# Performance work log

Hardware: AMD Instinct MI355X
Metric: run time of the kernel (lower is better)

The kernel has to match this reference:

```python
import jax, jax.numpy as jnp
import numpy as np

B, C, T, K = 16, 512, 2048, 64

def setup_inputs() -> dict:
    key = jax.random.key(0)
    k1, k2, k3 = jax.random.split(key, 3)
    v = jax.random.normal(k1, (B, C, T), dtype=jnp.float32)
    # 1x1 Conv1d weights == linear maps over channel dim
    Wk = jax.random.normal(k2, (K, C), dtype=jnp.float32) * 0.02
    bk = jnp.zeros((K,), dtype=jnp.float32)
    Wq = jax.random.normal(k3, (K, C), dtype=jnp.float32) * 0.02
    bq = jnp.zeros((K,), dtype=jnp.float32)
    gamma = jnp.ones((), dtype=jnp.float32)
    return {"v": v, "Wk": Wk, "bk": bk, "Wq": Wq, "bq": bq, "gamma": gamma}

def reference(v, Wk, bk, Wq, bq, gamma):
    # k, q: (B, K, T) via 1x1 conv = channel-wise linear
    k = jnp.einsum('kc,bct->bkt', Wk, v) + bk[None, :, None]
    q = jnp.einsum('kc,bct->bkt', Wq, v) + bq[None, :, None]
    # original: e1[b,d,i,j]=q[b,d,j], e2[b,d,i,j]=k[b,d,i]; sum over d
    # -> s[b,i,j] = sum_d k[b,d,i] * q[b,d,j]  (avoid materializing B,K,T,T)
    s = jnp.einsum('bdi,bdj->bij', k, q)  # (B, T, T)
    a = jax.nn.softmax(s, axis=1)          # softmax over dim=1 (the i axis)
    att = jnp.einsum('bct,btj->bcj', v, a)  # bmm(v, a)
    return v + gamma * att
```

## Files before the change

### kernel.cpp

```cpp
#include <hip/hip_runtime.h>

#define Bc 16
#define Cc 512
#define Tc 2048
#define QT 128
#define KT 64
#define PST 72
#define LTS 66

typedef __attribute__((ext_vector_type(8))) short short8;
typedef __attribute__((ext_vector_type(4))) float f32x4;
typedef unsigned short u16;

static __device__ __forceinline__ u16 f2bf(float x) {
  unsigned u = __float_as_uint(x);
  u += 0x7FFF + ((u >> 16) & 1);
  return (u16)(u >> 16);
}

static __device__ __forceinline__ void block_sync_lds() {
  __builtin_amdgcn_sched_barrier(0);
  asm volatile("s_waitcnt lgkmcnt(0)" ::: "memory");
  __builtin_amdgcn_s_barrier();
  __builtin_amdgcn_sched_barrier(0);
}

__global__ __launch_bounds__(256) void prep_kernel(
    const float* __restrict__ Wk, const float* __restrict__ Wq,
    const float* __restrict__ bk, const float* __restrict__ bq,
    u16* __restrict__ Wbf, float* __restrict__ bkq)
{
  int idx  = blockIdx.x * 256 + threadIdx.x;
  int base = idx * 4;
  if (base < 128 * Cc) {
    int ch = base >> 9;
    int c  = base & (Cc - 1);
    const float* src = (ch < 64) ? (Wk + (size_t)ch * Cc + c)
                                 : (Wq + (size_t)(ch - 64) * Cc + c);
    f32x4 w = *reinterpret_cast<const f32x4*>(src);
    uint2 o;
    o.x = (unsigned)f2bf(w[0]) | ((unsigned)f2bf(w[1]) << 16);
    o.y = (unsigned)f2bf(w[2]) | ((unsigned)f2bf(w[3]) << 16);
    *reinterpret_cast<uint2*>(Wbf + base) = o;
  }
  if (idx < 128) bkq[idx] = (idx < 64) ? bk[idx] : bq[idx - 64];
}

__global__ __launch_bounds__(256) void kqv_kernel(
    const float* __restrict__ v, const u16* __restrict__ Wbf,
    const float* __restrict__ bkq, u16* __restrict__ kq, u16* __restrict__ vbf)
{
  __shared__ u16 LDSt[2][64][LTS];
  const int b   = blockIdx.y;
  const int t0  = blockIdx.x * 64;
  const int tid = threadIdx.x;
  const int lane = tid & 63;
  const int w    = tid >> 6;
  const int l15  = lane & 15;
  const int lg   = lane >> 4;

  f32x4 acc[8];
  #pragma unroll
  for (int mt = 0; mt < 8; ++mt) acc[mt] = f32x4{0.f, 0.f, 0.f, 0.f};

  const float* vb = v + (size_t)b * Cc * Tc + t0;
  float x[16];
  #pragma unroll
  for (int r = 0; r < 16; ++r) x[r] = vb[(size_t)(w * 16 + r) * Tc + lane];

  int buf = 0;
  for (int c0 = 0; c0 < Cc; c0 += 64, buf ^= 1) {
    #pragma unroll
    for (int r = 0; r < 16; ++r) {
      u16 hb = f2bf(x[r]);
      LDSt[buf][lane][w * 16 + r] = hb;
      vbf[((size_t)b * Cc + c0 + w * 16 + r) * Tc + t0 + lane] = hb;
    }
    block_sync_lds();
    if (c0 + 64 < Cc) {
      #pragma unroll
      for (int r = 0; r < 16; ++r)
        x[r] = vb[(size_t)(c0 + 64 + w * 16 + r) * Tc + lane];
    }
    #pragma unroll
    for (int ks = 0; ks < 2; ++ks) {
      short8 bfrag = *reinterpret_cast<const short8*>(&LDSt[buf][w * 16 + l15][ks * 32 + lg * 8]);
      #pragma unroll
      for (int mt = 0; mt < 8; ++mt) {
        short8 afrag = *reinterpret_cast<const short8*>(
            Wbf + (size_t)(mt * 16 + l15) * Cc + c0 + ks * 32 + lg * 8);
        acc[mt] = __builtin_amdgcn_mfma_f32_16x16x32_bf16(afrag, bfrag, acc[mt], 0, 0, 0);
      }
    }
  }
  const int t = t0 + w * 16 + l15;
  u16* op = kq + ((size_t)b * Tc + t) * 128;
  #pragma unroll
  for (int mt = 0; mt < 8; ++mt) {
    int chb = mt * 16 + lg * 4;
    float a0 = acc[mt][0] + bkq[chb + 0];
    float a1 = acc[mt][1] + bkq[chb + 1];
    float a2 = acc[mt][2] + bkq[chb + 2];
    float a3 = acc[mt][3] + bkq[chb + 3];
    uint2 o;
    o.x = (unsigned)f2bf(a0) | ((unsigned)f2bf(a1) << 16);
    o.y = (unsigned)f2bf(a2) | ((unsigned)f2bf(a3) << 16);
    *reinterpret_cast<uint2*>(op + chb) = o;
  }
}

__global__ __launch_bounds__(512, 2) void attn_kernel(
    const float* __restrict__ v, const u16* __restrict__ vbf,
    const u16* __restrict__ kq, const float* __restrict__ gamma_p,
    float* __restrict__ out)
{
  __shared__ u16 P[2][QT * PST];
  __shared__ float scl_lds[2][QT];
  __shared__ float lsum_lds[QT];

  const int L   = blockIdx.x;
  const int lin = (L & 7) * 32 + (L >> 3);
  const int b   = lin >> 4;
  const int j0  = (lin & 15) * QT;
  const int tid = threadIdx.x;
  const int lane = tid & 63;
  const int wid  = tid >> 6;
  const int l15  = lane & 15;
  const int lg   = lane >> 4;
  const int c0   = wid * 64;

  short8 qf0, qf1;
  {
    const u16* qp = kq + (size_t)(b * Tc + j0 + wid * 16 + l15) * 128 + 64 + lg * 8;
    qf0 = *reinterpret_cast<const short8*>(qp);
    qf1 = *reinterpret_cast<const short8*>(qp + 32);
  }

  f32x4 O[4][8];
  #pragma unroll
  for (int a = 0; a < 4; ++a)
    #pragma unroll
    for (int bb = 0; bb < 8; ++bb) O[a][bb] = f32x4{0.f, 0.f, 0.f, 0.f};

  float m = -1e30f, lsum = 0.f;

  const u16* kbase = kq + (size_t)b * Tc * 128 + lg * 8;
  const u16* vbase = vbf + ((size_t)b * Cc + c0) * Tc;

  short8 kf[4][2];
  short8 vf[2][4];
  #pragma unroll
  for (int it = 0; it < 4; ++it) {
    const u16* kp = kbase + (size_t)(it * 16 + l15) * 128;
    kf[it][0] = *reinterpret_cast<const short8*>(kp);
    kf[it][1] = *reinterpret_cast<const short8*>(kp + 32);
  }
  #pragma unroll
  for (int is = 0; is < 2; ++is)
    #pragma unroll
    for (int ct = 0; ct < 4; ++ct)
      vf[is][ct] = *reinterpret_cast<const short8*>(
          vbase + (size_t)(ct * 16 + l15) * Tc + is * 32 + lg * 8);

  int pb = 0;
  for (int i0 = 0; i0 < Tc; i0 += KT, pb ^= 1) {
    f32x4 sacc[4];
    #pragma unroll
    for (int it = 0; it < 4; ++it) {
      f32x4 s = f32x4{0.f, 0.f, 0.f, 0.f};
      s = __builtin_amdgcn_mfma_f32_16x16x32_bf16(kf[it][0], qf0, s, 0, 0, 0);
      s = __builtin_amdgcn_mfma_f32_16x16x32_bf16(kf[it][1], qf1, s, 0, 0, 0);
      sacc[it] = s;
    }
    if (i0 + KT < Tc) {
      #pragma unroll
      for (int it = 0; it < 4; ++it) {
        const u16* kp = kbase + (size_t)(i0 + KT + it * 16 + l15) * 128;
        kf[it][0] = *reinterpret_cast<const short8*>(kp);
        kf[it][1] = *reinterpret_cast<const short8*>(kp + 32);
      }
    }

    float tmax = -1e30f;
    #pragma unroll
    for (int it = 0; it < 4; ++it)
      #pragma unroll
      for (int r = 0; r < 4; ++r) tmax = fmaxf(tmax, sacc[it][r]);
    tmax = fmaxf(tmax, __shfl_xor(tmax, 16));
    tmax = fmaxf(tmax, __shfl_xor(tmax, 32));
    bool defer  = (tmax - m <= 8.f);
    float mnew  = defer ? m : tmax;
    float scale = defer ? 1.f : __expf(m - tmax);
    float psum = 0.f;
    u16 pbv[4][4];
    #pragma unroll
    for (int it = 0; it < 4; ++it)
      #pragma unroll
      for (int r = 0; r < 4; ++r) {
        float p = __expf(sacc[it][r] - mnew);
        psum += p;
        pbv[it][r] = f2bf(p);
      }
    psum += __shfl_xor(psum, 16);
    psum += __shfl_xor(psum, 32);
    lsum = lsum * scale + psum;
    m = mnew;

    {
      u16* prow = &P[pb][(wid * 16 + l15) * PST];
      #pragma unroll
      for (int it = 0; it < 4; ++it) {
        uint2 wv;
        wv.x = (unsigned)pbv[it][0] | ((unsigned)pbv[it][1] << 16);
        wv.y = (unsigned)pbv[it][2] | ((unsigned)pbv[it][3] << 16);
        *reinterpret_cast<uint2*>(prow + it * 16 + lg * 4) = wv;
      }
    }
    if (lane < 16) scl_lds[pb][wid * 16 + lane] = scale;
    block_sync_lds();

    float sc[8];
    #pragma unroll
    for (int jj = 0; jj < 8; ++jj) sc[jj] = scl_lds[pb][jj * 16 + l15];
    bool need = false;
    #pragma unroll
    for (int jj = 0; jj < 8; ++jj) need |= (sc[jj] != 1.f);
    if (__any(need)) {
      #pragma unroll
      for (int ct = 0; ct < 4; ++ct)
        #pragma unroll
        for (int jj = 0; jj < 8; ++jj)
          #pragma unroll
          for (int r = 0; r < 4; ++r) O[ct][jj][r] *= sc[jj];
    }

    __builtin_amdgcn_s_setprio(1);
    #pragma unroll
    for (int is = 0; is < 2; ++is) {
      short8 pf[8];
      #pragma unroll
      for (int jj = 0; jj < 8; ++jj)
        pf[jj] = *reinterpret_cast<const short8*>(
            &P[pb][(jj * 16 + l15) * PST + is * 32 + lg * 8]);
      #pragma unroll
      for (int ct = 0; ct < 4; ++ct)
        #pragma unroll
        for (int jj = 0; jj < 8; ++jj)
          O[ct][jj] = __builtin_amdgcn_mfma_f32_16x16x32_bf16(vf[is][ct], pf[jj], O[ct][jj], 0, 0, 0);
    }
    __builtin_amdgcn_s_setprio(0);

    if (i0 + KT < Tc) {
      #pragma unroll
      for (int is = 0; is < 2; ++is)
        #pragma unroll
        for (int ct = 0; ct < 4; ++ct)
          vf[is][ct] = *reinterpret_cast<const short8*>(
              vbase + (size_t)(ct * 16 + l15) * Tc + (i0 + KT) + is * 32 + lg * 8);
    }
  }

  if (lane < 16) lsum_lds[wid * 16 + lane] = lsum;
  __syncthreads();
  const float gamma = *gamma_p;
  #pragma unroll
  for (int jj = 0; jj < 8; ++jj) {
    float linv = gamma / lsum_lds[jj * 16 + l15];
    int j = j0 + jj * 16 + l15;
    #pragma unroll
    for (int ct = 0; ct < 4; ++ct) {
      #pragma unroll
      for (int r = 0; r < 4; ++r) {
        int c = c0 + ct * 16 + lg * 4 + r;
        size_t idx = (size_t)(b * Cc + c) * Tc + j;
        out[idx] = v[idx] + linv * O[ct][jj][r];
      }
    }
  }
}

extern "C" void kernel_launch(void* const* d_in, const int* in_sizes, int n_in,
                              void* d_out, int out_size, void* d_ws, size_t ws_size,
                              hipStream_t stream) {
  const float* v  = (const float*)d_in[0];
  const float* Wk = (const float*)d_in[1];
  const float* bk = (const float*)d_in[2];
  const float* Wq = (const float*)d_in[3];
  const float* bq = (const float*)d_in[4];
  const float* gm = (const float*)d_in[5];
  float* out = (float*)d_out;

  char* ws = (char*)d_ws;
  u16*   kqb = (u16*)ws;
  u16*   vbf = (u16*)(ws + 8388608);
  u16*   Wbf = (u16*)(ws + 8388608 + 33554432);
  float* bkq = (float*)(ws + 8388608 + 33554432 + 131072);

  prep_kernel<<<dim3(64), dim3(256), 0, stream>>>(Wk, Wq, bk, bq, Wbf, bkq);
  kqv_kernel<<<dim3(Tc / 64, Bc), dim3(256), 0, stream>>>(v, Wbf, bkq, kqb, vbf);
  attn_kernel<<<dim3((Tc / QT) * Bc), dim3(512), 0, stream>>>(v, vbf, kqb, gm, out);
}
```

Before: 194.5 us.

## Shrink attention query tile to 64 with 4 waves covering 128 channels each

The query tile drops from 128 to 64 columns, the attention block shrinks from 8 to 4 waves, and each wave now owns 128 channels. This doubles the grid to 512 blocks and changes the block-to-batch mapping. The K fragments are no longer prefetched a tile ahead but loaded inline, and the second half of the V fragments is loaded after the barrier rather than prefetched. This trades cross-iteration prefetch and per-block reuse of K and V for more blocks and a different register footprint, so K/V global traffic per output roughly doubles.

```diff
diff --git a/kernel.cpp b/kernel.cpp
--- a/kernel.cpp
+++ b/kernel.cpp
@@ -3,7 +3,7 @@
 #define Bc 16
 #define Cc 512
 #define Tc 2048
-#define QT 128
+#define QT 64
 #define KT 64
 #define PST 72
 #define LTS 66
@@ -109,7 +109,7 @@
   }
 }
 
-__global__ __launch_bounds__(512, 2) void attn_kernel(
+__global__ __launch_bounds__(256, 2) void attn_kernel(
     const float* __restrict__ v, const u16* __restrict__ vbf,
     const u16* __restrict__ kq, const float* __restrict__ gamma_p,
     float* __restrict__ out)
@@ -119,15 +119,15 @@
   __shared__ float lsum_lds[QT];
 
   const int L   = blockIdx.x;
-  const int lin = (L & 7) * 32 + (L >> 3);
-  const int b   = lin >> 4;
-  const int j0  = (lin & 15) * QT;
+  const int lin = (L & 7) * 64 + (L >> 3);
+  const int b   = lin >> 5;
+  const int j0  = (lin & 31) * QT;
   const int tid = threadIdx.x;
   const int lane = tid & 63;
   const int wid  = tid >> 6;
   const int l15  = lane & 15;
   const int lg   = lane >> 4;
-  const int c0   = wid * 64;
+  const int c0   = wid * 128;
 
   short8 qf0, qf1;
   {
@@ -136,49 +136,35 @@
     qf1 = *reinterpret_cast<const short8*>(qp + 32);
   }
 
-  f32x4 O[4][8];
-  #pragma unroll
-  for (int a = 0; a < 4; ++a)
-    #pragma unroll
-    for (int bb = 0; bb < 8; ++bb) O[a][bb] = f32x4{0.f, 0.f, 0.f, 0.f};
+  f32x4 O[8][4];
+  #pragma unroll
+  for (int a = 0; a < 8; ++a)
+    #pragma unroll
+    for (int bb = 0; bb < 4; ++bb) O[a][bb] = f32x4{0.f, 0.f, 0.f, 0.f};
 
   float m = -1e30f, lsum = 0.f;
 
   const u16* kbase = kq + (size_t)b * Tc * 128 + lg * 8;
   const u16* vbase = vbf + ((size_t)b * Cc + c0) * Tc;
 
-  short8 kf[4][2];
-  short8 vf[2][4];
-  #pragma unroll
-  for (int it = 0; it < 4; ++it) {
-    const u16* kp = kbase + (size_t)(it * 16 + l15) * 128;
-    kf[it][0] = *reinterpret_cast<const short8*>(kp);
-    kf[it][1] = *reinterpret_cast<const short8*>(kp + 32);
-  }
-  #pragma unroll
-  for (int is = 0; is < 2; ++is)
-    #pragma unroll
-    for (int ct = 0; ct < 4; ++ct)
-      vf[is][ct] = *reinterpret_cast<const short8*>(
-          vbase + (size_t)(ct * 16 + l15) * Tc + is * 32 + lg * 8);
+  short8 vf0[8];
+  #pragma unroll
+  for (int ct = 0; ct < 8; ++ct)
+    vf0[ct] = *reinterpret_cast<const short8*>(
+        vbase + (size_t)(ct * 16 + l15) * Tc + lg * 8);
 
   int pb = 0;
   for (int i0 = 0; i0 < Tc; i0 += KT, pb ^= 1) {
     f32x4 sacc[4];
     #pragma unroll
     for (int it = 0; it < 4; ++it) {
+      const u16* kp = kbase + (size_t)(i0 + it * 16 + l15) * 128;
+      short8 af0 = *reinterpret_cast<const short8*>(kp);
+      short8 af1 = *reinterpret_cast<const short8*>(kp + 32);
       f32x4 s = f32x4{0.f, 0.f, 0.f, 0.f};
-      s = __builtin_amdgcn_mfma_f32_16x16x32_bf16(kf[it][0], qf0, s, 0, 0, 0);
-      s = __builtin_amdgcn_mfma_f32_16x16x32_bf16(kf[it][1], qf1, s, 0, 0, 0);
+      s = __builtin_amdgcn_mfma_f32_16x16x32_bf16(af0, qf0, s, 0, 0, 0);
+      s = __builtin_amdgcn_mfma_f32_16x16x32_bf16(af1, qf1, s, 0, 0, 0);
       sacc[it] = s;
-    }
-    if (i0 + KT < Tc) {
-      #pragma unroll
-      for (int it = 0; it < 4; ++it) {
-        const u16* kp = kbase + (size_t)(i0 + KT + it * 16 + l15) * 128;
-        kf[it][0] = *reinterpret_cast<const short8*>(kp);
-        kf[it][1] = *reinterpret_cast<const short8*>(kp + 32);
-      }
     }
 
     float tmax = -1e30f;
@@ -219,44 +205,59 @@
     if (lane < 16) scl_lds[pb][wid * 16 + lane] = scale;
     block_sync_lds();
 
-    float sc[8];
-    #pragma unroll
-    for (int jj = 0; jj < 8; ++jj) sc[jj] = scl_lds[pb][jj * 16 + l15];
+    short8 vf1[8];
+    #pragma unroll
+    for (int ct = 0; ct < 8; ++ct)
+      vf1[ct] = *reinterpret_cast<const short8*>(
+          vbase + (size_t)(ct * 16 + l15) * Tc + i0 + 32 + lg * 8);
+
+    float sc[4];
+    #pragma unroll
+    for (int jj = 0; jj < 4; ++jj) sc[jj] = scl_lds[pb][jj * 16 + l15];
     bool need = false;
     #pragma unroll
-    for (int jj = 0; jj < 8; ++jj) need |= (sc[jj] != 1.f);
+    for (int jj = 0; jj < 4; ++jj) need |= (sc[jj] != 1.f);
     if (__any(need)) {
       #pragma unroll
-      for (int ct = 0; ct < 4; ++ct)
+      for (int ct = 0; ct < 8; ++ct)
         #pragma unroll
-        for (int jj = 0; jj < 8; ++jj)
+        for (int jj = 0; jj < 4; ++jj)
           #pragma unroll
           for (int r = 0; r < 4; ++r) O[ct][jj][r] *= sc[jj];
     }
 
     __builtin_amdgcn_s_setprio(1);
-    #pragma unroll
-    for (int is = 0; is < 2; ++is) {
-      short8 pf[8];
-      #pragma unroll
-      for (int jj = 0; jj < 8; ++jj)
+    {
+      short8 pf[4];
+      #pragma unroll
+      for (int jj = 0; jj < 4; ++jj)
         pf[jj] = *reinterpret_cast<const short8*>(
-            &P[pb][(jj * 16 + l15) * PST + is * 32 + lg * 8]);
-      #pragma unroll
-      for (int ct = 0; ct < 4; ++ct)
+            &P[pb][(jj * 16 + l15) * PST + lg * 8]);
+      #pragma unroll
+      for (int ct = 0; ct < 8; ++ct)
         #pragma unroll
-        for (int jj = 0; jj < 8; ++jj)
-          O[ct][jj] = __builtin_amdgcn_mfma_f32_16x16x32_bf16(vf[is][ct], pf[jj], O[ct][jj], 0, 0, 0);
+        for (int jj = 0; jj < 4; ++jj)
+          O[ct][jj] = __builtin_amdgcn_mfma_f32_16x16x32_bf16(vf0[ct], pf[jj], O[ct][jj], 0, 0, 0);
+    }
+    {
+      short8 pf[4];
+      #pragma unroll
+      for (int jj = 0; jj < 4; ++jj)
+        pf[jj] = *reinterpret_cast<const short8*>(
+            &P[pb][(jj * 16 + l15) * PST + 32 + lg * 8]);
+      #pragma unroll
+      for (int ct = 0; ct < 8; ++ct)
+        #pragma unroll
+        for (int jj = 0; jj < 4; ++jj)
+          O[ct][jj] = __builtin_amdgcn_mfma_f32_16x16x32_bf16(vf1[ct], pf[jj], O[ct][jj], 0, 0, 0);
     }
     __builtin_amdgcn_s_setprio(0);
 
     if (i0 + KT < Tc) {
       #pragma unroll
-      for (int is = 0; is < 2; ++is)
-        #pragma unroll
-        for (int ct = 0; ct < 4; ++ct)
-          vf[is][ct] = *reinterpret_cast<const short8*>(
-              vbase + (size_t)(ct * 16 + l15) * Tc + (i0 + KT) + is * 32 + lg * 8);
+      for (int ct = 0; ct < 8; ++ct)
+        vf0[ct] = *reinterpret_cast<const short8*>(
+            vbase + (size_t)(ct * 16 + l15) * Tc + (i0 + KT) + lg * 8);
     }
   }
 
@@ -264,11 +265,11 @@
   __syncthreads();
   const float gamma = *gamma_p;
   #pragma unroll
-  for (int jj = 0; jj < 8; ++jj) {
+  for (int jj = 0; jj < 4; ++jj) {
     float linv = gamma / lsum_lds[jj * 16 + l15];
     int j = j0 + jj * 16 + l15;
     #pragma unroll
-    for (int ct = 0; ct < 4; ++ct) {
+    for (int ct = 0; ct < 8; ++ct) {
       #pragma unroll
       for (int r = 0; r < 4; ++r) {
         int c = c0 + ct * 16 + lg * 4 + r;
@@ -298,5 +299,5 @@
 
   prep_kernel<<<dim3(64), dim3(256), 0, stream>>>(Wk, Wq, bk, bq, Wbf, bkq);
   kqv_kernel<<<dim3(Tc / 64, Bc), dim3(256), 0, stream>>>(v, Wbf, bkq, kqb, vbf);
-  attn_kernel<<<dim3((Tc / QT) * Bc), dim3(512), 0, stream>>>(v, vbf, kqb, gm, out);
-}
+  attn_kernel<<<dim3((Tc / QT) * Bc), dim3(256), 0, stream>>>(v, vbf, kqb, gm, out);
+}
```

Result: slower. 260.5 us (+33.9%).
